# Performance work log

Hardware: AMD Instinct MI355X
Metric: run time of the kernel (lower is better)

Reference implementation:

```python
import jax, jax.numpy as jnp
import numpy as np

B, T, NIN = 128, 256, 16
H1 = H2 = 512
NACT = 4
SLOPE = 25.0  # snntorch FastSigmoid default slope

@jax.custom_vjp
def spike(x):
    return (x > 0).astype(x.dtype)

def _spike_fwd(x):
    return (x > 0).astype(x.dtype), x

def _spike_bwd(x, g):
    # FastSigmoid surrogate: d/dx = 1 / (slope*|x| + 1)^2
    return (g / (SLOPE * jnp.abs(x) + 1.0) ** 2,)

spike.defvjp(_spike_fwd, _spike_bwd)

def setup_inputs() -> dict:
    key = jax.random.key(0)
    ks = jax.random.split(key, 12)
    def lin(k, fan_in, shape):
        lim = 1.0 / np.sqrt(fan_in)
        return jax.random.uniform(k, shape, jnp.float32, -lim, lim)
    return {
        "batch": jax.random.uniform(ks[0], (B, T, NIN), jnp.float32, 0.0, 2.5),
        "W1": lin(ks[1], NIN, (H1, NIN)), "b1": lin(ks[2], NIN, (H1,)),
        "beta1": jax.random.uniform(ks[3], (H1,), jnp.float32),
        "thr1": jax.random.uniform(ks[4], (H1,), jnp.float32),
        "W2": lin(ks[5], H1, (H2, H1)), "b2": lin(ks[6], H1, (H2,)),
        "beta2": jax.random.uniform(ks[7], (H2,), jnp.float32),
        "thr2": jax.random.uniform(ks[8], (H2,), jnp.float32),
        "Wa": lin(ks[9], H2, (NACT, H2)), "ba": lin(ks[10], H2, (NACT,)),
        "beta_act": jnp.float32(0.95),
        "inp_min": jnp.float32(0.0),
        "inp_max": jnp.float32(2.5),
    }

def _lif_subtract(cur, mem, beta, thr):
    # snntorch Leaky: reset from PRE-update membrane, detached; subtract reset
    reset = jax.lax.stop_gradient((mem - thr > 0).astype(mem.dtype))
    mem = jnp.clip(beta, 0.0, 1.0) * mem + cur - reset * thr
    return spike(mem - thr), mem

def reference(batch, W1, b1, beta1, thr1, W2, b2, beta2, thr2, Wa, ba, beta_act, inp_min, inp_max):
    Bb = batch.shape[0]
    x_seq = jnp.swapaxes(batch, 0, 1)  # [T, B, NIN]
    mem1 = jnp.zeros((Bb, W1.shape[0]), batch.dtype)
    mem2 = jnp.zeros((Bb, W2.shape[0]), batch.dtype)
    mem_a = jnp.zeros((Bb, Wa.shape[0]), batch.dtype)

    def step(carry, x):
        mem1, mem2, mem_a = carry
        x = (x - inp_min) / (inp_max - inp_min)
        spk1, mem1 = _lif_subtract(x @ W1.T + b1, mem1, beta1, thr1)
        spk2, mem2 = _lif_subtract(spk1 @ W2.T + b2, mem2, beta2, thr2)
        act = spk2 @ Wa.T + ba
        # action_lif: reset_mechanism='none', beta=0.95 learnable
        mem_a = jnp.clip(beta_act, 0.0, 1.0) * mem_a + act
        return (mem1, mem2, mem_a), mem_a.reshape(-1)  # torch: mem_act.reshape((1,-1))

    _, vals = jax.lax.scan(step, (mem1, mem2, mem_a), x_seq)
    # torch.stack(values, dim=1) of (1, B*NACT) tensors -> (1, T, B*NACT)
    return vals[None, :, :]
```

## Files before the change

kernel.cpp:

```cpp
#include <hip/hip_runtime.h>
#include <stdint.h>

typedef __attribute__((ext_vector_type(8))) short short8;
typedef __attribute__((ext_vector_type(4))) float f32x4;

#define T_STEPS 256
#define BATCH   128

#define LDS_BARRIER() asm volatile("s_waitcnt lgkmcnt(0)\n\ts_barrier" ::: "memory")

static __device__ inline unsigned short f2bf(float f) {
    unsigned int u = __float_as_uint(f);
    unsigned int r = u + 0x7FFFu + ((u >> 16) & 1u);
    return (unsigned short)(r >> 16);
}
static __device__ inline unsigned pack_hi16(unsigned a, unsigned b) {
    return (a >> 16) | (b & 0xFFFF0000u);
}

__global__ __launch_bounds__(256) void k_prep(
    const float* __restrict__ W2, const float* __restrict__ W1,
    const float* __restrict__ b1, const float* __restrict__ thr1,
    const float* __restrict__ imin_p, const float* __restrict__ imax_p,
    const float* __restrict__ batch,
    unsigned short* __restrict__ W2hi, unsigned short* __restrict__ W2lo,
    unsigned short* __restrict__ W1rows, float* __restrict__ b1s,
    unsigned short* __restrict__ Xf)
{
    int blk = blockIdx.x, tid = threadIdx.x;
    if (blk < 256) {
        int gid = blk * 256 + tid;
        f32x4 wv = *(const f32x4*)(W2 + (size_t)gid * 4);
        unsigned short hi[4], lo[4];
#pragma unroll
        for (int e = 0; e < 4; ++e) {
            float wf = wv[e];
            unsigned short h = f2bf(wf);
            float hf = __uint_as_float(((unsigned int)h) << 16);
            hi[e] = h;
            lo[e] = f2bf(wf - hf);
        }
        uint2 ph, pl;
        ph.x = (unsigned)hi[0] | ((unsigned)hi[1] << 16);
        ph.y = (unsigned)hi[2] | ((unsigned)hi[3] << 16);
        pl.x = (unsigned)lo[0] | ((unsigned)lo[1] << 16);
        pl.y = (unsigned)lo[2] | ((unsigned)lo[3] << 16);
        *(uint2*)(W2hi + (size_t)gid * 4) = ph;
        *(uint2*)(W2lo + (size_t)gid * 4) = pl;
    } else if (blk < 258) {
        int h = (blk - 256) * 256 + tid;
        float wsc = 1.0f / thr1[h];
        unsigned short row[64];
#pragma unroll
        for (int k = 0; k < 16; ++k) {
            float wv = W1[h * 16 + k] * wsc;
            unsigned a = __float_as_uint(wv) & 0xFFFF0000u;
            float r1 = wv - __uint_as_float(a);
            unsigned m = __float_as_uint(r1) & 0xFFFF0000u;
            float r2 = r1 - __uint_as_float(m);
            unsigned l = __float_as_uint(r2) & 0xFFFF0000u;
            row[k]      = (unsigned short)(a >> 16);
            row[16 + k] = (unsigned short)(m >> 16);
            row[32 + k] = (unsigned short)(l >> 16);
            row[48 + k] = 0;
        }
        b1s[h] = b1[h] * wsc;
        uint4* dst = (uint4*)(W1rows + (size_t)h * 64);
#pragma unroll
        for (int i = 0; i < 8; ++i) dst[i] = ((uint4*)row)[i];
    } else {
        int gid   = (blk - 258) * 256 + tid;
        int lane  = gid & 63;
        int btile = (gid >> 6) & 7;
        int t     = gid >> 9;
        int q     = lane >> 4, m15 = lane & 15;
        int b     = btile * 16 + m15;
        float imin = imin_p[0];
        float isc  = 1.0f / (imax_p[0] - imin);
        const float* xp = batch + ((size_t)b * T_STEPS + t) * 16 + (q & 1) * 8;
        unsigned uh[8], um[8], ul[8];
#pragma unroll
        for (int j = 0; j < 8; ++j) {
            float xv = (xp[j] - imin) * isc;
            unsigned a = __float_as_uint(xv) & 0xFFFF0000u;
            float r1 = xv - __uint_as_float(a);
            unsigned m = __float_as_uint(r1) & 0xFFFF0000u;
            float r2 = r1 - __uint_as_float(m);
            unsigned l = __float_as_uint(r2) & 0xFFFF0000u;
            uh[j] = a; um[j] = m; ul[j] = l;
        }
        uint4 B1, B2, XL;
        B1.x = pack_hi16(uh[0], uh[1]); B1.y = pack_hi16(uh[2], uh[3]);
        B1.z = pack_hi16(uh[4], uh[5]); B1.w = pack_hi16(uh[6], uh[7]);
        B2.x = pack_hi16(um[0], um[1]); B2.y = pack_hi16(um[2], um[3]);
        B2.z = pack_hi16(um[4], um[5]); B2.w = pack_hi16(um[6], um[7]);
        XL.x = pack_hi16(ul[0], ul[1]); XL.y = pack_hi16(ul[2], ul[3]);
        XL.z = pack_hi16(ul[4], ul[5]); XL.w = pack_hi16(ul[6], ul[7]);
        uint4 B3 = (q < 2) ? XL : B1;
        uint4 B4 = (q < 2) ? XL : B2;
        unsigned short* dst = Xf + (((size_t)t * 8 + btile) * 4) * 512 + lane * 8;
        *(uint4*)(dst +    0) = B1;
        *(uint4*)(dst +  512) = B2;
        *(uint4*)(dst + 1024) = B3;
        *(uint4*)(dst + 1536) = B4;
    }
}

__global__ __launch_bounds__(1024, 4) void k_main(
    const unsigned short* __restrict__ Xf,
    const unsigned short* __restrict__ W2hi, const unsigned short* __restrict__ W2lo,
    const unsigned short* __restrict__ W1rows, const float* __restrict__ b1s,
    const float* __restrict__ beta1, const float* __restrict__ b2,
    const float* __restrict__ beta2, const float* __restrict__ thr2,
    unsigned short* __restrict__ spkbits)
{
    __shared__ unsigned short Aw[8192];
    __shared__ float Cbuf[2][4096];

    int tid  = threadIdx.x;
    int lane = tid & 63;
    int w    = tid >> 6;
    int q    = lane >> 4, m15 = lane & 15;
    int btile = blockIdx.x & 7;
    int slice = blockIdx.x >> 3;

    short8 A1[2], A2[2], A3[2];
#pragma unroll
    for (int c = 0; c < 2; ++c) {
        const unsigned short* rp = W1rows + (size_t)(w * 32 + c * 16 + m15) * 64;
        A1[c] = *(const short8*)(rp + q * 8);
        A2[c] = *(const short8*)(rp + q * 8 + (q >> 1) * 16);
        A3[c] = *(const short8*)(rp + 16 + q * 8);
    }
    int jg = slice * 16 + m15;
    short8 bhi = *(const short8*)(W2hi + (size_t)jg * 512 + w * 32 + q * 8);
    short8 blo = *(const short8*)(W2lo + (size_t)jg * 512 + w * 32 + q * 8);

    f32x4 b14[2], bet1[2];
#pragma unroll
    for (int c = 0; c < 2; ++c) {
        int h0 = w * 32 + c * 16 + q * 4;
        b14[c] = *(const f32x4*)(b1s + h0);
        f32x4 bb = *(const f32x4*)(beta1 + h0);
#pragma unroll
        for (int r = 0; r < 4; ++r) bet1[c][r] = fminf(fmaxf(bb[r], 0.0f), 1.0f);
    }
    float m1[8], spk1f[8];
#pragma unroll
    for (int i = 0; i < 8; ++i) { m1[i] = 0.0f; spk1f[i] = 0.0f; }

    float beta2r = fminf(fmaxf(beta2[jg], 0.0f), 1.0f);
    float thr2r  = thr2[jg];
    float nthr2  = -thr2r;
    float b2r    = b2[jg];
    float m2 = 0.0f, spk2f = 0.0f;

    const unsigned short* xbase = Xf + ((size_t)btile * 4) * 512 + lane * 8;
    uint4 xc[4], xn[4];
#pragma unroll
    for (int f = 0; f < 4; ++f) xc[f] = *(const uint4*)(xbase + f * 512);

    unsigned short* myAw = Aw + w * 512;
    int wr0 = (0 * 2 + (q >> 1)) * 128 + (m15 ^ (q >> 1)) * 8 + (q & 1) * 4;
    int wr1 = (1 * 2 + (q >> 1)) * 128 + (m15 ^ (q >> 1)) * 8 + (q & 1) * 4;
    int rdo = (q * 16 + (m15 ^ (q & 1))) * 8;

    auto body = [&](int ts, uint4* xcur, uint4* xnx) __attribute__((always_inline)) {
        int buf = ts & 1;
        int tn = (ts + 1 < T_STEPS) ? ts + 1 : ts;
        const unsigned short* xp = xbase + (size_t)tn * 16384;
#pragma unroll
        for (int f = 0; f < 4; ++f) xnx[f] = *(const uint4*)(xp + f * 512);

        union { uint4 u; short8 s; } Bf[4];
#pragma unroll
        for (int f = 0; f < 4; ++f) Bf[f].u = xcur[f];
        f32x4 D[2];
#pragma unroll
        for (int c = 0; c < 2; ++c) {
            D[c] = b14[c];
            D[c] = __builtin_amdgcn_mfma_f32_16x16x32_bf16(A1[c], Bf[0].s, D[c], 0, 0, 0);
            D[c] = __builtin_amdgcn_mfma_f32_16x16x32_bf16(A1[c], Bf[1].s, D[c], 0, 0, 0);
            D[c] = __builtin_amdgcn_mfma_f32_16x16x32_bf16(A2[c], Bf[2].s, D[c], 0, 0, 0);
            D[c] = __builtin_amdgcn_mfma_f32_16x16x32_bf16(A3[c], Bf[3].s, D[c], 0, 0, 0);
        }
#pragma unroll
        for (int i = 0; i < 8; ++i) {
            int c = i >> 2, r = i & 3;
            float mv = fmaf(bet1[c][r], m1[i], D[c][r]);
            mv -= spk1f[i];
            bool sp = mv > 1.0f;
            m1[i] = mv;
            spk1f[i] = sp ? 1.0f : 0.0f;
        }
        {
            uint2 pk0, pk1;
            pk0.x = pack_hi16(__float_as_uint(spk1f[0]), __float_as_uint(spk1f[1]));
            pk0.y = pack_hi16(__float_as_uint(spk1f[2]), __float_as_uint(spk1f[3]));
            pk1.x = pack_hi16(__float_as_uint(spk1f[4]), __float_as_uint(spk1f[5]));
            pk1.y = pack_hi16(__float_as_uint(spk1f[6]), __float_as_uint(spk1f[7]));
            *(uint2*)(myAw + wr0) = pk0;
            *(uint2*)(myAw + wr1) = pk1;
        }
        union { uint4 u; short8 s; } af;
        af.u = *(uint4*)(myAw + rdo);
        f32x4 C2 = { 0.f, 0.f, 0.f, 0.f };
        C2 = __builtin_amdgcn_mfma_f32_16x16x32_bf16(af.s, bhi, C2, 0, 0, 0);
        C2 = __builtin_amdgcn_mfma_f32_16x16x32_bf16(af.s, blo, C2, 0, 0, 0);
#pragma unroll
        for (int r = 0; r < 4; ++r)
            Cbuf[buf][r * 1024 + w * 64 + lane] = C2[r];
        LDS_BARRIER();
        if (w < 4) {
            float cur2 = b2r;
#pragma unroll
            for (int wp = 0; wp < 16; ++wp) cur2 += Cbuf[buf][w * 1024 + wp * 64 + lane];
            m2 = fmaf(beta2r, m2, cur2);
            m2 = fmaf(spk2f, nthr2, m2);
            bool sp2 = m2 > thr2r;
            spk2f = sp2 ? 1.0f : 0.0f;
            unsigned long long mask = __ballot(sp2);
            if (lane < 4) {
                unsigned short v = (unsigned short)(mask >> (lane * 16));
                spkbits[((size_t)ts * BATCH + btile * 16 + lane * 4 + w) * 32 + slice] = v;
            }
        }
    };

#pragma unroll 1
    for (int ts = 0; ts < T_STEPS; ts += 2) {
        body(ts, xc, xn);
        body(ts + 1, xn, xc);
    }
}

__global__ __launch_bounds__(256) void k_act(
    const unsigned short* __restrict__ spkbits,
    const float* __restrict__ Wa, const float* __restrict__ ba,
    const float* __restrict__ beta_act_p, float* __restrict__ out)
{
    __shared__ f32x4 waT[512];
    __shared__ f32x4 sc[256];
    int tid = threadIdx.x;
    int b   = blockIdx.x;

    for (int j = tid; j < 512; j += 256) {
        f32x4 v = { Wa[j], Wa[512 + j], Wa[1024 + j], Wa[1536 + j] };
        waT[j] = v;
    }
    float bact = fminf(fmaxf(beta_act_p[0], 0.0f), 1.0f);
    f32x4 acc = { ba[0], ba[1], ba[2], ba[3] };
    __syncthreads();

    const unsigned short* sp = spkbits + ((size_t)tid * BATCH + b) * 32;
    unsigned int wbuf[16];
#pragma unroll
    for (int r = 0; r < 4; ++r) {
        uint4 v = *(const uint4*)(sp + r * 8);
        wbuf[r*4+0] = v.x; wbuf[r*4+1] = v.y; wbuf[r*4+2] = v.z; wbuf[r*4+3] = v.w;
    }
    for (int s = 0; s < 32; ++s) {
        unsigned int wd = (wbuf[s >> 1] >> ((s & 1) * 16)) & 0xFFFFu;
#pragma unroll
        for (int i = 0; i < 16; ++i) {
            float sel = ((wd >> i) & 1u) ? 1.0f : 0.0f;
            f32x4 wv = waT[s * 16 + i];
            acc[0] = fmaf(sel, wv[0], acc[0]);
            acc[1] = fmaf(sel, wv[1], acc[1]);
            acc[2] = fmaf(sel, wv[2], acc[2]);
            acc[3] = fmaf(sel, wv[3], acc[3]);
        }
    }
    sc[tid] = acc;
    __syncthreads();
    float bd = bact;
    for (int d = 1; d < 256; d <<= 1) {
        f32x4 cv = sc[tid];
        f32x4 pv = { 0.f, 0.f, 0.f, 0.f };
        if (tid >= d) pv = sc[tid - d];
        __syncthreads();
        cv[0] = fmaf(bd, pv[0], cv[0]);
        cv[1] = fmaf(bd, pv[1], cv[1]);
        cv[2] = fmaf(bd, pv[2], cv[2]);
        cv[3] = fmaf(bd, pv[3], cv[3]);
        sc[tid] = cv;
        __syncthreads();
        bd *= bd;
    }
    f32x4 res = sc[tid];
    *(f32x4*)(out + (size_t)tid * 512 + b * 4) = res;
}

extern "C" void kernel_launch(void* const* d_in, const int* in_sizes, int n_in,
                              void* d_out, int out_size, void* d_ws, size_t ws_size,
                              hipStream_t stream)
{
    const float* batch    = (const float*)d_in[0];
    const float* W1       = (const float*)d_in[1];
    const float* b1       = (const float*)d_in[2];
    const float* beta1    = (const float*)d_in[3];
    const float* thr1     = (const float*)d_in[4];
    const float* W2       = (const float*)d_in[5];
    const float* b2       = (const float*)d_in[6];
    const float* beta2    = (const float*)d_in[7];
    const float* thr2     = (const float*)d_in[8];
    const float* Wa       = (const float*)d_in[9];
    const float* ba       = (const float*)d_in[10];
    const float* beta_act = (const float*)d_in[11];
    const float* inp_min  = (const float*)d_in[12];
    const float* inp_max  = (const float*)d_in[13];
    float* out            = (float*)d_out;

    char* ws = (char*)d_ws;
    unsigned short* W2hi    = (unsigned short*)ws;
    unsigned short* W2lo    = (unsigned short*)(ws + (512u << 10));
    unsigned short* W1rows  = (unsigned short*)(ws + (1u << 20));
    float*          b1s     = (float*)(ws + (1u << 20) + (64u << 10));
    unsigned short* Xf      = (unsigned short*)(ws + (2u << 20));
    unsigned short* spkbits = (unsigned short*)(ws + (10u << 20));

    hipLaunchKernelGGL(k_prep, dim3(770), dim3(256), 0, stream,
                       W2, W1, b1, thr1, inp_min, inp_max, batch,
                       W2hi, W2lo, W1rows, b1s, Xf);
    hipLaunchKernelGGL(k_main, dim3(256), dim3(1024), 0, stream,
                       Xf, W2hi, W2lo, W1rows, b1s, beta1, b2, beta2, thr2, spkbits);
    hipLaunchKernelGGL(k_act, dim3(128), dim3(256), 0, stream, spkbits, Wa, ba, beta_act, out);
}
```

Before: 310.0 us.

## Stage input fragments in LDS via async global-to-LDS loads by one wave

The prep kernel now stores only the three bf16 split planes of each input (hi, mid, lo) instead of four duplicated MFMA fragments, which shrinks the Xf buffer and the number of prep blocks. In the main kernel, one wave fetches each timestep's input tile two steps ahead into a 4-slot LDS ring using global_load_lds, and all waves read their fragments from LDS. This replaces the per-wave redundant global loads, trading them for LDS reads and an extra vmcnt wait before the existing barrier. pack_hi16 also now uses a single byte-permute instruction.

Measured after the change: 289.0 us. 1.07x faster.

```diff
diff --git a/kernel.cpp b/kernel.cpp
--- a/kernel.cpp
+++ b/kernel.cpp
@@ -15,7 +15,13 @@
     return (unsigned short)(r >> 16);
 }
 static __device__ inline unsigned pack_hi16(unsigned a, unsigned b) {
-    return (a >> 16) | (b & 0xFFFF0000u);
+    return __builtin_amdgcn_perm(b, a, 0x07060302u);
+}
+static __device__ inline void gload_lds16(const unsigned short* g, unsigned short* l) {
+    __builtin_amdgcn_global_load_lds(
+        (const __attribute__((address_space(1))) unsigned int*)(const void*)g,
+        (__attribute__((address_space(3))) unsigned int*)(void*)l,
+        16, 0, 0);
 }
 
 __global__ __launch_bounds__(256) void k_prep(
@@ -69,15 +75,15 @@
 #pragma unroll
         for (int i = 0; i < 8; ++i) dst[i] = ((uint4*)row)[i];
     } else {
-        int gid   = (blk - 258) * 256 + tid;
-        int lane  = gid & 63;
-        int btile = (gid >> 6) & 7;
-        int t     = gid >> 9;
-        int q     = lane >> 4, m15 = lane & 15;
-        int b     = btile * 16 + m15;
+        int gid    = (blk - 258) * 256 + tid;
+        int lane32 = gid & 31;
+        int btile  = (gid >> 5) & 7;
+        int t      = gid >> 8;
+        int q1 = lane32 >> 4, m15 = lane32 & 15;
+        int b  = btile * 16 + m15;
         float imin = imin_p[0];
         float isc  = 1.0f / (imax_p[0] - imin);
-        const float* xp = batch + ((size_t)b * T_STEPS + t) * 16 + (q & 1) * 8;
+        const float* xp = batch + ((size_t)b * T_STEPS + t) * 16 + q1 * 8;
         unsigned uh[8], um[8], ul[8];
 #pragma unroll
         for (int j = 0; j < 8; ++j) {
@@ -89,22 +95,21 @@
             unsigned l = __float_as_uint(r2) & 0xFFFF0000u;
             uh[j] = a; um[j] = m; ul[j] = l;
         }
-        uint4 B1, B2, XL;
-        B1.x = pack_hi16(uh[0], uh[1]); B1.y = pack_hi16(uh[2], uh[3]);
-        B1.z = pack_hi16(uh[4], uh[5]); B1.w = pack_hi16(uh[6], uh[7]);
-        B2.x = pack_hi16(um[0], um[1]); B2.y = pack_hi16(um[2], um[3]);
-        B2.z = pack_hi16(um[4], um[5]); B2.w = pack_hi16(um[6], um[7]);
+        uint4 XH, XM, XL;
+        XH.x = pack_hi16(uh[0], uh[1]); XH.y = pack_hi16(uh[2], uh[3]);
+        XH.z = pack_hi16(uh[4], uh[5]); XH.w = pack_hi16(uh[6], uh[7]);
+        XM.x = pack_hi16(um[0], um[1]); XM.y = pack_hi16(um[2], um[3]);
+        XM.z = pack_hi16(um[4], um[5]); XM.w = pack_hi16(um[6], um[7]);
         XL.x = pack_hi16(ul[0], ul[1]); XL.y = pack_hi16(ul[2], ul[3]);
         XL.z = pack_hi16(ul[4], ul[5]); XL.w = pack_hi16(ul[6], ul[7]);
-        uint4 B3 = (q < 2) ? XL : B1;
-        uint4 B4 = (q < 2) ? XL : B2;
-        unsigned short* dst = Xf + (((size_t)t * 8 + btile) * 4) * 512 + lane * 8;
-        *(uint4*)(dst +    0) = B1;
-        *(uint4*)(dst +  512) = B2;
-        *(uint4*)(dst + 1024) = B3;
-        *(uint4*)(dst + 1536) = B4;
-    }
-}
+        unsigned short* dst = Xf + ((size_t)t * 8 + btile) * 1024 + lane32 * 8;
+        *(uint4*)(dst +   0) = XH;
+        *(uint4*)(dst + 256) = XM;
+        *(uint4*)(dst + 512) = XL;
+    }
+}
+
+union XF { uint4 u; short8 s; };
 
 __global__ __launch_bounds__(1024, 4) void k_main(
     const unsigned short* __restrict__ Xf,
@@ -116,11 +121,12 @@
 {
     __shared__ unsigned short Aw[8192];
     __shared__ float Cbuf[2][4096];
+    __shared__ unsigned short Xs[4096];
 
     int tid  = threadIdx.x;
     int lane = tid & 63;
     int w    = tid >> 6;
-    int q    = lane >> 4, m15 = lane & 15;
+    int q = lane >> 4, m15 = lane & 15;
     int btile = blockIdx.x & 7;
     int slice = blockIdx.x >> 3;
 
@@ -155,34 +161,60 @@
     float b2r    = b2[jg];
     float m2 = 0.0f, spk2f = 0.0f;
 
-    const unsigned short* xbase = Xf + ((size_t)btile * 4) * 512 + lane * 8;
-    uint4 xc[4], xn[4];
-#pragma unroll
-    for (int f = 0; f < 4; ++f) xc[f] = *(const uint4*)(xbase + f * 512);
+    const unsigned short* xgbase = Xf + (size_t)btile * 1024 + (size_t)lane * 8;
+    int l31x8 = (lane & 31) * 8;
+    int o1 = l31x8;
+    int o2 = l31x8 + 256;
+    int o3 = l31x8 + (lane < 32 ? 512 : 0);
+    int o4 = l31x8 + (lane < 32 ? 512 : 256);
 
     unsigned short* myAw = Aw + w * 512;
     int wr0 = (0 * 2 + (q >> 1)) * 128 + (m15 ^ (q >> 1)) * 8 + (q & 1) * 4;
     int wr1 = (1 * 2 + (q >> 1)) * 128 + (m15 ^ (q >> 1)) * 8 + (q & 1) * 4;
     int rdo = (q * 16 + (m15 ^ (q & 1))) * 8;
 
-    auto body = [&](int ts, uint4* xcur, uint4* xnx) __attribute__((always_inline)) {
+    if (w == 15) {
+        gload_lds16(xgbase,              Xs);
+        gload_lds16(xgbase + 512,        Xs + 512);
+        gload_lds16(xgbase + 8192,       Xs + 1024);
+        gload_lds16(xgbase + 8192 + 512, Xs + 1536);
+        asm volatile("s_waitcnt vmcnt(0)" ::: "memory");
+    }
+    __syncthreads();
+
+    XF xc[4], xn[4];
+    {
+        const unsigned short* s = Xs;
+        xc[0].u = *(const uint4*)(s + o1);
+        xc[1].u = *(const uint4*)(s + o2);
+        xc[2].u = *(const uint4*)(s + o3);
+        xc[3].u = *(const uint4*)(s + o4);
+    }
+
+    auto body = [&](int ts, XF* xcur, XF* xnx) __attribute__((always_inline)) {
         int buf = ts & 1;
-        int tn = (ts + 1 < T_STEPS) ? ts + 1 : ts;
-        const unsigned short* xp = xbase + (size_t)tn * 16384;
-#pragma unroll
-        for (int f = 0; f < 4; ++f) xnx[f] = *(const uint4*)(xp + f * 512);
-
-        union { uint4 u; short8 s; } Bf[4];
-#pragma unroll
-        for (int f = 0; f < 4; ++f) Bf[f].u = xcur[f];
+        if (w == 15) {
+            int t2 = (ts + 2 < T_STEPS) ? ts + 2 : T_STEPS - 1;
+            const unsigned short* g = xgbase + (size_t)t2 * 8192;
+            unsigned short* l = Xs + (((ts + 2) & 3) << 10);
+            gload_lds16(g,       l);
+            gload_lds16(g + 512, l + 512);
+        }
+        {
+            const unsigned short* s = Xs + (((ts + 1) & 3) << 10);
+            xnx[0].u = *(const uint4*)(s + o1);
+            xnx[1].u = *(const uint4*)(s + o2);
+            xnx[2].u = *(const uint4*)(s + o3);
+            xnx[3].u = *(const uint4*)(s + o4);
+        }
+
         f32x4 D[2];
 #pragma unroll
         for (int c = 0; c < 2; ++c) {
-            D[c] = b14[c];
-            D[c] = __builtin_amdgcn_mfma_f32_16x16x32_bf16(A1[c], Bf[0].s, D[c], 0, 0, 0);
-            D[c] = __builtin_amdgcn_mfma_f32_16x16x32_bf16(A1[c], Bf[1].s, D[c], 0, 0, 0);
-            D[c] = __builtin_amdgcn_mfma_f32_16x16x32_bf16(A2[c], Bf[2].s, D[c], 0, 0, 0);
-            D[c] = __builtin_amdgcn_mfma_f32_16x16x32_bf16(A3[c], Bf[3].s, D[c], 0, 0, 0);
+            D[c] = __builtin_amdgcn_mfma_f32_16x16x32_bf16(A1[c], xcur[0].s, b14[c], 0, 0, 0);
+            D[c] = __builtin_amdgcn_mfma_f32_16x16x32_bf16(A1[c], xcur[1].s, D[c], 0, 0, 0);
+            D[c] = __builtin_amdgcn_mfma_f32_16x16x32_bf16(A2[c], xcur[2].s, D[c], 0, 0, 0);
+            D[c] = __builtin_amdgcn_mfma_f32_16x16x32_bf16(A3[c], xcur[3].s, D[c], 0, 0, 0);
         }
 #pragma unroll
         for (int i = 0; i < 8; ++i) {
@@ -210,6 +242,7 @@
 #pragma unroll
         for (int r = 0; r < 4; ++r)
             Cbuf[buf][r * 1024 + w * 64 + lane] = C2[r];
+        if (w == 15) asm volatile("s_waitcnt vmcnt(0)" ::: "memory");
         LDS_BARRIER();
         if (w < 4) {
             float cur2 = b2r;
@@ -319,7 +352,7 @@
     unsigned short* Xf      = (unsigned short*)(ws + (2u << 20));
     unsigned short* spkbits = (unsigned short*)(ws + (10u << 20));
 
-    hipLaunchKernelGGL(k_prep, dim3(770), dim3(256), 0, stream,
+    hipLaunchKernelGGL(k_prep, dim3(514), dim3(256), 0, stream,
                        W2, W1, b1, thr1, inp_min, inp_max, batch,
                        W2hi, W2lo, W1rows, b1s, Xf);
     hipLaunchKernelGGL(k_main, dim3(256), dim3(1024), 0, stream,
```
